# Kernel tuning notes

Measured on AMD Instinct MI355X. Metric: run time of the kernel, lower is better.

Reference implementation:

```python
import jax, jax.numpy as jnp
import numpy as np

B, DAYS, N, E = 2, 8, 10000, 80000
C_IN, C_OUT, H = 32, 32, 4
NEG_SLOPE = 0.2


def setup_inputs() -> dict:
    key = jax.random.key(0)
    ks = jax.random.split(key, 7)
    x = jax.random.randint(ks[0], (B, DAYS, N), 0, N)
    adjacency = jax.random.randint(ks[1], (2, E), 0, N)
    embedding = jax.random.normal(ks[2], (N, C_IN), dtype=jnp.float32)
    # GATConv linear: in_channels -> heads*out_channels
    W = jax.random.normal(ks[3], (C_IN, H * C_OUT), dtype=jnp.float32) / np.sqrt(C_IN)
    att_src = jax.random.normal(ks[4], (H, C_OUT), dtype=jnp.float32) / np.sqrt(C_OUT)
    att_dst = jax.random.normal(ks[5], (H, C_OUT), dtype=jnp.float32) / np.sqrt(C_OUT)
    bias = jnp.zeros((H * C_OUT,), dtype=jnp.float32)
    return {"x": x, "adjacency": adjacency, "embedding": embedding,
            "W": W, "att_src": att_src, "att_dst": att_dst, "bias": bias}


def _gat_forward(feat, src, dst, W, att_src, att_dst, bias):
    # feat: [G, N, C_IN]; same edge list shared across the G graphs
    G = feat.shape[0]
    xh = (feat @ W).reshape(G, N, H, C_OUT)              # [G,N,H,C]
    a_src = jnp.einsum('gnhc,hc->gnh', xh, att_src)       # [G,N,H]
    a_dst = jnp.einsum('gnhc,hc->gnh', xh, att_dst)
    alpha = a_src[:, src] + a_dst[:, dst]                 # [G,Et,H]
    alpha = jnp.where(alpha >= 0, alpha, NEG_SLOPE * alpha)

    def per_graph(al, msgs):
        # segment softmax over incoming edges of each dst node
        m = jax.ops.segment_max(al, dst, num_segments=N)  # [N,H]
        e = jnp.exp(al - m[dst])                          # [Et,H]
        s = jax.ops.segment_sum(e, dst, num_segments=N)
        w = e / (s[dst] + 1e-16)
        out = jax.ops.segment_sum(w[..., None] * msgs, dst, num_segments=N)
        return out                                        # [N,H,C]

    out = jax.vmap(per_graph)(alpha, xh[:, src])          # [G,N,H,C]
    return out.reshape(G, N, H * C_OUT) + bias


def reference(x, adjacency, embedding, W, att_src, att_dst, bias):
    Bd, Dd = x.shape[0], x.shape[1]
    feat = embedding[x].reshape(-1, N, C_IN)              # [G,N,C_IN]
    # GATConv default add_self_loops=True
    loops = jnp.arange(N, dtype=adjacency.dtype)
    src = jnp.concatenate([adjacency[0], loops])
    dst = jnp.concatenate([adjacency[1], loops])
    out = _gat_forward(feat, src, dst, W, att_src, att_dst, bias)
    return out.reshape(Bd, Dd, -1)
```

## Files before the change

kernel.cpp:

```cpp
#include <hip/hip_runtime.h>
#include <hip/hip_bf16.h>
#include <math.h>

#define C_IN 32
#define H 4
#define C_OUT 32
#define HC (H * C_OUT)
#define NEG_SLOPE 0.2f
#define CSR_STRIDE 64

typedef float v2f __attribute__((ext_vector_type(2)));

#define RPB 16
__global__ __launch_bounds__(256) void build_kernel(
        const int* __restrict__ adj, int E, int N,
        int* __restrict__ deg, int* __restrict__ csr,
        const float* __restrict__ emb, const float* __restrict__ W,
        const float* __restrict__ att_src, const float* __restrict__ att_dst,
        __hip_bfloat16* __restrict__ T, float* __restrict__ ta_src,
        float* __restrict__ ta_dst, int tblocks) {
    if ((int)blockIdx.x >= tblocks) {
        int e = (blockIdx.x - tblocks) * 256 + threadIdx.x;
        int Et = E + N;
        if (e < Et) {
            int s = (e < E) ? adj[e] : (e - E);
            int d = (e < E) ? adj[E + e] : (e - E);
            int pos = atomicAdd(&deg[d], 1);
            if (pos < CSR_STRIDE) csr[(d << 6) + pos] = s;
        }
        return;
    }
    int t = threadIdx.x;
    int sub = t >> 7;
    int tc = t & 127;
    int h = tc >> 5, c = tc & 31;
    int base = blockIdx.x * RPB;
    int nmax = (N - base < RPB) ? (N - base) : RPB;

    float wcol[C_IN];
#pragma unroll
    for (int k = 0; k < C_IN; k++) wcol[k] = W[k * HC + tc];
    float as = att_src[h * C_OUT + c];
    float adw = att_dst[h * C_OUT + c];

    for (int it = sub; it < nmax; it += 2) {
        int r = __builtin_amdgcn_readfirstlane(base + it);
        const float* ep = emb + (size_t)r * C_IN;
        float acc = 0.f;
#pragma unroll
        for (int k = 0; k < C_IN; k++) acc += ep[k] * wcol[k];
        T[(size_t)r * HC + tc] = __float2bfloat16(acc);
        float ps = acc * as, pd = acc * adw;
#pragma unroll
        for (int o = 16; o; o >>= 1) {
            ps += __shfl_xor(ps, o, 32);
            pd += __shfl_xor(pd, o, 32);
        }
        if (c == 0) {
            ta_src[r * H + h] = ps;
            ta_dst[r * H + h] = pd;
        }
    }
}

__global__ __launch_bounds__(256) void agg_kernel(
        const int* __restrict__ deg, const int* __restrict__ csr,
        const int* __restrict__ x, const unsigned int* __restrict__ Tu,
        const float* __restrict__ ta_src, const float* __restrict__ ta_dst,
        const float* __restrict__ bias, float* __restrict__ out, int N, int G) {
    __shared__ float w_lds[CSR_STRIDE][16][4];
    __shared__ int   xs8_lds[16][65];
    __shared__ float ds_lds[16][4];

    int t = threadIdx.x;
    int n = blockIdx.x;
    int dg = deg[n];
    if (dg > CSR_STRIDE) dg = CSR_STRIDE;
    int dgp4 = (dg + 3) & ~3;
    const int* cb = csr + (n << 6);

    {
        int g = t >> 4;
        int e0 = t & 15;
        const int* xg = x + (size_t)g * N;
        for (int c0 = 0; c0 < dg; c0 += 16) {
            int slot = c0 + e0;
            int sv = cb[slot];
            int s = (slot < dg) ? sv : 0;
            xs8_lds[g][slot] = xg[s] << 8;
        }
    }
    __syncthreads();

    {
        int g = t >> 4;
        int es = (t >> 2) & 3;
        int h = t & 3;
        int xgn = x[(size_t)g * N + n];
        float adv = ta_dst[xgn * H + h];
        float dpart = 0.f;
        for (int c0 = 0; c0 < dgp4; c0 += 4) {
            int slot = c0 + es;
            int xs = xs8_lds[g][slot] >> 8;
            float a = ta_src[xs * H + h] + adv;
            a = fmaxf(a, NEG_SLOPE * a);
            float w = (slot < dg) ? __expf(a) : 0.f;
            w_lds[slot][g][h] = w;
            dpart += w;
        }
        dpart += __shfl_xor(dpart, 4, 64);
        dpart += __shfl_xor(dpart, 8, 64);
        if (es == 0) ds_lds[g][h] = dpart;
    }
    __syncthreads();

    int wid = t >> 6;
    int lane = t & 63;
    int lg = lane >> 4;
    int li = lane & 15;
    int gj = wid * 4 + lg;
    int hh = li >> 2;
    unsigned int li16 = (unsigned int)(li << 4);

    v2f a0 = {0.f, 0.f}, a1 = {0.f, 0.f}, a2 = {0.f, 0.f}, a3 = {0.f, 0.f};

#pragma unroll 4
    for (int e = 0; e < dgp4; e++) {
        unsigned int off = (unsigned int)xs8_lds[gj][e] + li16;
        float w = w_lds[e][gj][hh];
        uint4 u = *(const uint4*)((const char*)Tu + off);
        a0.x += w * __uint_as_float(u.x << 16);
        a0.y += w * __uint_as_float(u.x & 0xffff0000u);
        a1.x += w * __uint_as_float(u.y << 16);
        a1.y += w * __uint_as_float(u.y & 0xffff0000u);
        a2.x += w * __uint_as_float(u.z << 16);
        a2.y += w * __uint_as_float(u.z & 0xffff0000u);
        a3.x += w * __uint_as_float(u.w << 16);
        a3.y += w * __uint_as_float(u.w & 0xffff0000u);
    }

    float inv = __builtin_amdgcn_rcpf(ds_lds[gj][hh] + 1e-16f);
    const float4* bp = (const float4*)(bias + li * 8);
    float4 b0 = bp[0], b1 = bp[1];
    float4 o0 = {a0.x * inv + b0.x, a0.y * inv + b0.y,
                 a1.x * inv + b0.z, a1.y * inv + b0.w};
    float4 o1 = {a2.x * inv + b1.x, a2.y * inv + b1.y,
                 a3.x * inv + b1.z, a3.y * inv + b1.w};
    float* op = out + (size_t)gj * N * HC + (size_t)n * HC + li * 8;
    *(float4*)op = o0;
    *(float4*)(op + 4) = o1;
}

extern "C" void kernel_launch(void* const* d_in, const int* in_sizes, int n_in,
                              void* d_out, int out_size, void* d_ws, size_t ws_size,
                              hipStream_t stream) {
    const int*   x       = (const int*)d_in[0];
    const int*   adj     = (const int*)d_in[1];
    const float* emb     = (const float*)d_in[2];
    const float* W       = (const float*)d_in[3];
    const float* att_src = (const float*)d_in[4];
    const float* att_dst = (const float*)d_in[5];
    const float* bias    = (const float*)d_in[6];
    float* out = (float*)d_out;

    const int N  = in_sizes[2] / C_IN;
    const int GN = in_sizes[0];
    const int G  = GN / N;
    const int E  = in_sizes[1] / 2;
    const int Et = E + N;

    char* ws = (char*)d_ws;
    size_t o = 0;
    auto carve = [&](size_t bytes) -> void* {
        void* p = ws + o;
        o = (o + bytes + 255) & ~(size_t)255;
        return p;
    };
    __hip_bfloat16* T = (__hip_bfloat16*)carve((size_t)N * HC * sizeof(__hip_bfloat16));
    float* ta_src  = (float*)carve((size_t)N * H * sizeof(float));
    float* ta_dst  = (float*)carve((size_t)N * H * sizeof(float));
    int*   deg     = (int*)carve((size_t)N * sizeof(int));
    int*   csr     = (int*)carve((size_t)N * CSR_STRIDE * sizeof(int));

    hipMemsetAsync(deg, 0, (size_t)N * sizeof(int), stream);

    int tblocks = (N + RPB - 1) / RPB;
    int fblocks = (Et + 255) / 256;
    build_kernel<<<tblocks + fblocks, 256, 0, stream>>>(
        adj, E, N, deg, csr, emb, W, att_src, att_dst, T, ta_src, ta_dst, tblocks);

    agg_kernel<<<N, 256, 0, stream>>>(deg, csr, x,
                                      (const unsigned int*)T, ta_src, ta_dst,
                                      bias, out, N, G);
}
```

Measured before the change: 149.3 us.

## Make aggregation kernel grid-stride over nodes and use packed v2f FMAs

```diff
diff --git a/kernel.cpp b/kernel.cpp
--- a/kernel.cpp
+++ b/kernel.cpp
@@ -73,47 +73,11 @@
     __shared__ float ds_lds[16][4];
 
     int t = threadIdx.x;
-    int n = blockIdx.x;
-    int dg = deg[n];
-    if (dg > CSR_STRIDE) dg = CSR_STRIDE;
-    int dgp4 = (dg + 3) & ~3;
-    const int* cb = csr + (n << 6);
-
-    {
-        int g = t >> 4;
-        int e0 = t & 15;
-        const int* xg = x + (size_t)g * N;
-        for (int c0 = 0; c0 < dg; c0 += 16) {
-            int slot = c0 + e0;
-            int sv = cb[slot];
-            int s = (slot < dg) ? sv : 0;
-            xs8_lds[g][slot] = xg[s] << 8;
-        }
-    }
-    __syncthreads();
-
-    {
-        int g = t >> 4;
-        int es = (t >> 2) & 3;
-        int h = t & 3;
-        int xgn = x[(size_t)g * N + n];
-        float adv = ta_dst[xgn * H + h];
-        float dpart = 0.f;
-        for (int c0 = 0; c0 < dgp4; c0 += 4) {
-            int slot = c0 + es;
-            int xs = xs8_lds[g][slot] >> 8;
-            float a = ta_src[xs * H + h] + adv;
-            a = fmaxf(a, NEG_SLOPE * a);
-            float w = (slot < dg) ? __expf(a) : 0.f;
-            w_lds[slot][g][h] = w;
-            dpart += w;
-        }
-        dpart += __shfl_xor(dpart, 4, 64);
-        dpart += __shfl_xor(dpart, 8, 64);
-        if (es == 0) ds_lds[g][h] = dpart;
-    }
-    __syncthreads();
-
+
+    int gA = t >> 4;
+    int e0 = t & 15;
+    int es = (t >> 2) & 3;
+    int hB = t & 3;
     int wid = t >> 6;
     int lane = t & 63;
     int lg = lane >> 4;
@@ -121,34 +85,78 @@
     int gj = wid * 4 + lg;
     int hh = li >> 2;
     unsigned int li16 = (unsigned int)(li << 4);
-
-    v2f a0 = {0.f, 0.f}, a1 = {0.f, 0.f}, a2 = {0.f, 0.f}, a3 = {0.f, 0.f};
-
-#pragma unroll 4
-    for (int e = 0; e < dgp4; e++) {
-        unsigned int off = (unsigned int)xs8_lds[gj][e] + li16;
-        float w = w_lds[e][gj][hh];
-        uint4 u = *(const uint4*)((const char*)Tu + off);
-        a0.x += w * __uint_as_float(u.x << 16);
-        a0.y += w * __uint_as_float(u.x & 0xffff0000u);
-        a1.x += w * __uint_as_float(u.y << 16);
-        a1.y += w * __uint_as_float(u.y & 0xffff0000u);
-        a2.x += w * __uint_as_float(u.z << 16);
-        a2.y += w * __uint_as_float(u.z & 0xffff0000u);
-        a3.x += w * __uint_as_float(u.w << 16);
-        a3.y += w * __uint_as_float(u.w & 0xffff0000u);
-    }
-
-    float inv = __builtin_amdgcn_rcpf(ds_lds[gj][hh] + 1e-16f);
     const float4* bp = (const float4*)(bias + li * 8);
     float4 b0 = bp[0], b1 = bp[1];
-    float4 o0 = {a0.x * inv + b0.x, a0.y * inv + b0.y,
-                 a1.x * inv + b0.z, a1.y * inv + b0.w};
-    float4 o1 = {a2.x * inv + b1.x, a2.y * inv + b1.y,
-                 a3.x * inv + b1.z, a3.y * inv + b1.w};
-    float* op = out + (size_t)gj * N * HC + (size_t)n * HC + li * 8;
-    *(float4*)op = o0;
-    *(float4*)(op + 4) = o1;
+
+    for (int n = blockIdx.x; n < N; n += gridDim.x) {
+        int dg = deg[n];
+        if (dg > CSR_STRIDE) dg = CSR_STRIDE;
+        int dgp4 = (dg + 3) & ~3;
+        const int* cb = csr + (n << 6);
+
+        {
+            const int* xg = x + (size_t)gA * N;
+            for (int c0 = 0; c0 < dg; c0 += 16) {
+                int slot = c0 + e0;
+                int sv = cb[slot];
+                int s = (slot < dg) ? sv : 0;
+                xs8_lds[gA][slot] = xg[s] << 8;
+            }
+        }
+        __syncthreads();
+
+        {
+            int xgn = x[(size_t)gA * N + n];
+            float adv = ta_dst[xgn * H + hB];
+            float dpart = 0.f;
+            for (int c0 = 0; c0 < dgp4; c0 += 4) {
+                int slot = c0 + es;
+                int xs = xs8_lds[gA][slot] >> 8;
+                float a = ta_src[xs * H + hB] + adv;
+                a = fmaxf(a, NEG_SLOPE * a);
+                float w = (slot < dg) ? __expf(a) : 0.f;
+                w_lds[slot][gA][hB] = w;
+                dpart += w;
+            }
+            dpart += __shfl_xor(dpart, 4, 64);
+            dpart += __shfl_xor(dpart, 8, 64);
+            if (es == 0) ds_lds[gA][hB] = dpart;
+        }
+        __syncthreads();
+
+        v2f a0 = {0.f, 0.f}, a1 = {0.f, 0.f}, a2 = {0.f, 0.f}, a3 = {0.f, 0.f};
+
+#pragma unroll 4
+        for (int e = 0; e < dgp4; e++) {
+            unsigned int off = (unsigned int)xs8_lds[gj][e] + li16;
+            float w = w_lds[e][gj][hh];
+            v2f w2 = {w, w};
+            uint4 u = *(const uint4*)((const char*)Tu + off);
+            v2f t0 = {__uint_as_float(u.x << 16),
+                      __uint_as_float(u.x & 0xffff0000u)};
+            v2f t1 = {__uint_as_float(u.y << 16),
+                      __uint_as_float(u.y & 0xffff0000u)};
+            v2f t2 = {__uint_as_float(u.z << 16),
+                      __uint_as_float(u.z & 0xffff0000u)};
+            v2f t3 = {__uint_as_float(u.w << 16),
+                      __uint_as_float(u.w & 0xffff0000u)};
+            a0 += w2 * t0;
+            a1 += w2 * t1;
+            a2 += w2 * t2;
+            a3 += w2 * t3;
+        }
+
+        float inv = __builtin_amdgcn_rcpf(ds_lds[gj][hh] + 1e-16f);
+        float4 o0 = {a0.x * inv + b0.x, a0.y * inv + b0.y,
+                     a1.x * inv + b0.z, a1.y * inv + b0.w};
+        float4 o1 = {a2.x * inv + b1.x, a2.y * inv + b1.y,
+                     a3.x * inv + b1.z, a3.y * inv + b1.w};
+        float* op = out + (size_t)gj * N * HC + (size_t)n * HC + li * 8;
+        *(float4*)op = o0;
+        *(float4*)(op + 4) = o1;
+
+        __syncthreads();
+    }
 }
 
 extern "C" void kernel_launch(void* const* d_in, const int* in_sizes, int n_in,
@@ -189,7 +197,8 @@
     build_kernel<<<tblocks + fblocks, 256, 0, stream>>>(
         adj, E, N, deg, csr, emb, W, att_src, att_dst, T, ta_src, ta_dst, tblocks);
 
-    agg_kernel<<<N, 256, 0, stream>>>(deg, csr, x,
-                                      (const unsigned int*)T, ta_src, ta_dst,
-                                      bias, out, N, G);
+    int ablocks = (N + 3) / 4;
+    agg_kernel<<<ablocks, 256, 0, stream>>>(deg, csr, x,
+                                            (const unsigned int*)T, ta_src, ta_dst,
+                                            bias, out, N, G);
 }
```

Result: slower. 152.5 us (+2.1%).
